# Performance work log

Measured on AMD Instinct MI355X. Metric: run time of the kernel, lower is better.

## Reference

```python
import jax, jax.numpy as jnp
import numpy as np

N_NODES = 100000
N_EDGES = 1600000
IN_F = 128
N_HEADS = 8
HEAD_D = 8  # n_hidden // n_heads = 64 // 8
NEG_SLOPE = 0.2


def setup_inputs() -> dict:
    key = jax.random.key(0)
    k1, k2, k3, k4, k5 = jax.random.split(key, 5)
    vert = jax.random.normal(k1, (N_NODES, IN_F), dtype=jnp.float32)
    edge = jax.random.randint(k2, (2, N_EDGES), 0, N_NODES, dtype=jnp.int64)
    scale_w = 1.0 / np.sqrt(IN_F)
    W = jax.random.normal(k3, (IN_F, N_HEADS, HEAD_D), dtype=jnp.float32) * scale_w
    scale_a = 1.0 / np.sqrt(HEAD_D)
    a_src = jax.random.normal(k4, (N_HEADS, HEAD_D), dtype=jnp.float32) * scale_a
    a_dst = jax.random.normal(k5, (N_HEADS, HEAD_D), dtype=jnp.float32) * scale_a
    return {"vert": vert, "edge": edge, "W": W, "a_src": a_src, "a_dst": a_dst}


def reference(vert, edge, W, a_src, a_dst):
    # Per-head linear projection: [N, H, D]
    g = jnp.einsum('nf,fhd->nhd', vert, W)
    src, dst = edge[0], edge[1]
    # Decomposed attention logits: e_ij = LeakyReLU(a_src.g_i + a_dst.g_j)
    e_s = jnp.sum(g * a_src[None], axis=-1)  # [N, H]
    e_d = jnp.sum(g * a_dst[None], axis=-1)  # [N, H]
    scores = jax.nn.leaky_relu(e_s[src] + e_d[dst], NEG_SLOPE)  # [E, H]
    # Segment softmax over incoming edges of each destination node
    m = jax.ops.segment_max(scores, dst, num_segments=N_NODES)  # [N, H]
    m = jnp.where(jnp.isneginf(m), 0.0, m)
    ex = jnp.exp(scores - m[dst])  # [E, H]
    denom = jax.ops.segment_sum(ex, dst, num_segments=N_NODES)  # [N, H]
    alpha = ex / jnp.maximum(denom[dst], 1e-16)  # [E, H]
    # Weighted message aggregation: scatter-add alpha * g[src] into dst
    msg = alpha[:, :, None] * g[src]  # [E, H, D]
    agg = jax.ops.segment_sum(msg, dst, num_segments=N_NODES)  # [N, H, D]
    out = agg.reshape(N_NODES, N_HEADS * HEAD_D)  # concat heads
    # GAT_DE trailing ELU (dropout=0.0 -> identity)
    return jax.nn.elu(out)
```

## Files before the change

kernel.cpp:

```cpp
#include <hip/hip_runtime.h>
#include <hip/hip_bf16.h>
#include <math.h>

#define N_NODES 100000
#define N_EDGES 1600000
#define IN_F    128
#define NH      8
#define HD      8
#define HID     64
#define NEG_SLOPE 0.2f

#define BSH   5
#define BSZ   32
#define NBK   3125
#define BCAPG 704
#define BCAP  832
#define NBPJ  782
#define NPB   160
#define EPB   10000

typedef short bf16x8 __attribute__((ext_vector_type(8)));
typedef float f32x4  __attribute__((ext_vector_type(4)));

static __device__ __forceinline__ unsigned short f2bf(float x) {
    __hip_bfloat16 h = __float2bfloat16(x);
    return *(unsigned short*)&h;
}

__global__ __launch_bounds__(512) void fused_pp_kernel(
    const float* __restrict__ vert, const float* __restrict__ W,
    const float* __restrict__ a_src, const float* __restrict__ a_dst,
    __hip_bfloat16* __restrict__ gb, float* __restrict__ es, float* __restrict__ ed,
    const int* __restrict__ edge, int* __restrict__ gcnt,
    unsigned int* __restrict__ packed)
{
    __shared__ __align__(16) char smem[25088];
    const int tid = threadIdx.x;

    if (blockIdx.x < NBPJ) {
        unsigned short* b_lds = (unsigned short*)smem;
        const int nbeg = blockIdx.x * 128;
        const int lane = tid & 63, wv = tid >> 6;
        const int mn   = lane & 15, quad = lane >> 4;

        for (int idx = tid; idx < 128 * 16; idx += 512) {
            const int f = idx >> 4, cq = idx & 15;
            const float4 w = *(const float4*)(W + f * 64 + cq * 4);
            const int kc = f >> 5, q = (f >> 3) & 3, j = f & 7;
            const float wf[4] = {w.x, w.y, w.z, w.w};
            #pragma unroll
            for (int i = 0; i < 4; ++i) {
                const int col = cq * 4 + i;
                b_lds[(col >> 4) * 2048 + kc * 512 + q * 128 + (col & 15) * 8 + j]
                    = f2bf(wf[i]);
            }
        }
        for (int idx = tid; idx < 128 * 8; idx += 512) {
            const int f = idx >> 3, h = idx & 7;
            const float4 wa = *(const float4*)(W + f * 64 + h * 8);
            const float4 wb = *(const float4*)(W + f * 64 + h * 8 + 4);
            const float4 sa = *(const float4*)(a_src + h * 8);
            const float4 sb = *(const float4*)(a_src + h * 8 + 4);
            const float4 da = *(const float4*)(a_dst + h * 8);
            const float4 db = *(const float4*)(a_dst + h * 8 + 4);
            float esv = fmaf(wa.x, sa.x, fmaf(wa.y, sa.y, fmaf(wa.z, sa.z,
                        fmaf(wa.w, sa.w, fmaf(wb.x, sb.x, fmaf(wb.y, sb.y,
                        fmaf(wb.z, sb.z, wb.w * sb.w)))))));
            float edv = fmaf(wa.x, da.x, fmaf(wa.y, da.y, fmaf(wa.z, da.z,
                        fmaf(wa.w, da.w, fmaf(wb.x, db.x, fmaf(wb.y, db.y,
                        fmaf(wb.z, db.z, wb.w * db.w)))))));
            const int kc = f >> 5, q = (f >> 3) & 3, j = f & 7;
            b_lds[4 * 2048 + kc * 512 + q * 128 + h * 8 + j]       = f2bf(esv);
            b_lds[4 * 2048 + kc * 512 + q * 128 + (8 + h) * 8 + j] = f2bf(edv);
        }

        const int row = nbeg + wv * 16 + mn;
        bf16x8 afr[4];
        #pragma unroll
        for (int kc = 0; kc < 4; ++kc) {
            float4 p = make_float4(0.f, 0.f, 0.f, 0.f);
            float4 q4 = make_float4(0.f, 0.f, 0.f, 0.f);
            if (row < N_NODES) {
                const float* rp = vert + (size_t)row * IN_F + kc * 32 + quad * 8;
                p  = *(const float4*)rp;
                q4 = *(const float4*)(rp + 4);
            }
            bf16x8 a;
            a[0] = (short)f2bf(p.x);  a[1] = (short)f2bf(p.y);
            a[2] = (short)f2bf(p.z);  a[3] = (short)f2bf(p.w);
            a[4] = (short)f2bf(q4.x); a[5] = (short)f2bf(q4.y);
            a[6] = (short)f2bf(q4.z); a[7] = (short)f2bf(q4.w);
            afr[kc] = a;
        }
        __syncthreads();

        const unsigned short* bbase = b_lds + quad * 128 + mn * 8;
        f32x4 acc[5];
        #pragma unroll
        for (int c = 0; c < 5; ++c) acc[c] = (f32x4){0.f, 0.f, 0.f, 0.f};
        #pragma unroll
        for (int kc = 0; kc < 4; ++kc) {
            #pragma unroll
            for (int c = 0; c < 5; ++c) {
                const bf16x8 bfr = *(const bf16x8*)(bbase + c * 2048 + kc * 512);
                acc[c] = __builtin_amdgcn_mfma_f32_16x16x32_bf16(afr[kc], bfr, acc[c], 0, 0, 0);
            }
        }
        __syncthreads();

        unsigned short* gl = (unsigned short*)smem + wv * 1024;
        float* lesd = (float*)(smem + 16384) + wv * 256;
        #pragma unroll
        for (int c = 0; c < 4; ++c)
            #pragma unroll
            for (int r = 0; r < 4; ++r)
                gl[(quad * 4 + r) * 64 + c * 16 + mn] = f2bf(acc[c][r]);
        {
            float* dst = (mn < 8) ? (lesd + mn) : (lesd + 128 + (mn - 8));
            #pragma unroll
            for (int r = 0; r < 4; ++r) dst[(quad * 4 + r) * 8] = acc[4][r];
        }
        {
            const int row2 = lane >> 2, part = lane & 3;
            const int node = nbeg + wv * 16 + row2;
            if (node < N_NODES) {
                const uint4* sp = (const uint4*)(gl + row2 * 64 + part * 16);
                *(uint4*)((unsigned short*)gb + (size_t)node * HID + part * 16) = sp[0];
                *(uint4*)((unsigned short*)gb + (size_t)node * HID + part * 16 + 8) = sp[1];
            }
        }
        {
            const int nl = lane >> 2, h2 = (lane & 3) * 2;
            const int node = nbeg + wv * 16 + nl;
            if (node < N_NODES) {
                *(float2*)(es + node * NH + h2) = *(const float2*)(lesd + nl * 8 + h2);
                *(float2*)(ed + node * NH + h2) = *(const float2*)(lesd + 128 + nl * 8 + h2);
            }
        }
    } else {
        int* lh    = (int*)smem;
        int* lbase = (int*)(smem + 12544);
        const int pb = blockIdx.x - NBPJ;

        for (int i = tid; i < NBK; i += 512) lh[i] = 0;
        __syncthreads();
        const int4* src4 = (const int4*)(edge + pb * EPB);
        const int4* dst4 = (const int4*)(edge + N_EDGES + pb * EPB);
        for (int t = tid; t < EPB / 4; t += 512) {
            const int4 d = dst4[t];
            atomicAdd(&lh[d.x >> BSH], 1);
            atomicAdd(&lh[d.y >> BSH], 1);
            atomicAdd(&lh[d.z >> BSH], 1);
            atomicAdd(&lh[d.w >> BSH], 1);
        }
        __syncthreads();
        for (int i = tid; i < NBK; i += 512) {
            const int c = lh[i];
            lbase[i] = c ? (i * BCAPG + atomicAdd(&gcnt[i], c)) : 0;
            lh[i] = 0;
        }
        __syncthreads();
        for (int t = tid; t < EPB / 4; t += 512) {
            const int4 s = src4[t];
            const int4 d = dst4[t];
            int bk, pos;
            bk = d.x >> BSH; pos = min(lbase[bk] + atomicAdd(&lh[bk], 1), NBK * BCAPG - 1);
            packed[pos] = ((unsigned)s.x << BSH) | (d.x & (BSZ - 1));
            bk = d.y >> BSH; pos = min(lbase[bk] + atomicAdd(&lh[bk], 1), NBK * BCAPG - 1);
            packed[pos] = ((unsigned)s.y << BSH) | (d.y & (BSZ - 1));
            bk = d.z >> BSH; pos = min(lbase[bk] + atomicAdd(&lh[bk], 1), NBK * BCAPG - 1);
            packed[pos] = ((unsigned)s.z << BSH) | (d.z & (BSZ - 1));
            bk = d.w >> BSH; pos = min(lbase[bk] + atomicAdd(&lh[bk], 1), NBK * BCAPG - 1);
            packed[pos] = ((unsigned)s.w << BSH) | (d.w & (BSZ - 1));
        }
    }
}

__global__ __launch_bounds__(256) void p2agg_kernel(
    const int* __restrict__ gcnt, const unsigned int* __restrict__ packed,
    const unsigned short* __restrict__ gb, const float* __restrict__ es,
    const float* __restrict__ ed, float* __restrict__ out)
{
    __shared__ unsigned int epk[BCAP];
    __shared__ unsigned int ssrt[BCAP];
    __shared__ int ldeg[BSZ], loffs[BSZ];
    __shared__ float led[BSZ * NH];

    const int tid  = threadIdx.x;
    const int b    = blockIdx.x;
    const int nbeg = b << BSH;
    const int ebase = b * BCAPG;
    const int ecnt  = min(gcnt[b], BCAP);

    if (tid < BSZ) ldeg[tid] = 0;
    for (int i = tid; i < BSZ * NH; i += 256) led[i] = ed[nbeg * NH + i];
    __syncthreads();

    for (int i = tid; i < ecnt; i += 256) {
        const unsigned int p = packed[ebase + i];
        epk[i] = p;
        atomicAdd(&ldeg[p & (BSZ - 1)], 1);
    }
    __syncthreads();

    if (tid < BSZ) {
        int v = ldeg[tid];
        #pragma unroll
        for (int off = 1; off < BSZ; off <<= 1) {
            const int t = __shfl_up(v, off, 64);
            if (tid >= off) v += t;
        }
        loffs[tid] = v - ldeg[tid];
    }
    __syncthreads();

    for (int i = tid; i < ecnt; i += 256) {
        const unsigned int p = epk[i];
        const int pos = atomicAdd(&loffs[p & (BSZ - 1)], 1);
        ssrt[pos] = p >> BSH;
    }
    __syncthreads();

    const int lane  = tid & 63;
    const int wv    = tid >> 6;
    const int h     = lane >> 3;
    const int d8    = lane & 7;
    const int c2    = lane & 31;
    const int khalf = lane >> 5;
    const int bpbase = ((c2 >> 2) * 8 + khalf) * 4;
    const unsigned* gbw = (const unsigned*)gb;

    for (int n = wv; n < BSZ; n += 4) {
        const int node = nbeg + n;
        const float edh = led[n * NH + h];
        const int end = loffs[n];
        const int beg = end - ldeg[n];
        float l = 0.f, acc0 = 0.f, acc1 = 0.f;
        for (int i = beg; i < end; i += 8) {
            const int idx = min(i + d8, end - 1);
            const int sd  = (int)ssrt[idx];
            float sc = es[sd * NH + h] + edh;
            sc = fmaxf(sc, sc * NEG_SLOPE);
            const float pd = (i + d8 < end) ? __expf(sc) : 0.f;
            #pragma unroll
            for (int s = 0; s < 4; ++s) {
                const int a  = bpbase + s * 8;
                const int se = __builtin_amdgcn_ds_bpermute(a, sd);
                const float pe = __uint_as_float((unsigned)
                    __builtin_amdgcn_ds_bpermute(a, __float_as_int(pd)));
                const unsigned gu = gbw[(unsigned)(se * 32 + c2)];
                acc0 = fmaf(pe, __uint_as_float(gu << 16), acc0);
                acc1 = fmaf(pe, __uint_as_float(gu & 0xFFFF0000u), acc1);
                l += pe;
            }
        }
        l    += __shfl_xor(l, 32);
        acc0 += __shfl_xor(acc0, 32);
        acc1 += __shfl_xor(acc1, 32);
        const float rl = 1.f / fmaxf(l, 1e-16f);
        float o0 = acc0 * rl, o1 = acc1 * rl;
        o0 = (o0 > 0.f) ? o0 : expm1f(o0);
        o1 = (o1 > 0.f) ? o1 : expm1f(o1);
        const float ov = khalf ? o1 : o0;
        out[(size_t)node * HID + c2 * 2 + khalf] = ov;
    }
}

extern "C" void kernel_launch(void* const* d_in, const int* in_sizes, int n_in,
                              void* d_out, int out_size, void* d_ws, size_t ws_size,
                              hipStream_t stream)
{
    const float* vert  = (const float*)d_in[0];
    const int*   edge  = (const int*)  d_in[1];
    const float* W     = (const float*)d_in[2];
    const float* a_src = (const float*)d_in[3];
    const float* a_dst = (const float*)d_in[4];
    float* out = (float*)d_out;

    char* ws = (char*)d_ws;
    __hip_bfloat16* gb     = (__hip_bfloat16*)(ws);
    float*          es     = (float*)(ws + 12800000);
    float*          ed     = (float*)(ws + 16000000);
    unsigned int*   packed = (unsigned int*)(ws + 19200000);
    int*            gcnt   = (int*)(ws + 28000000);

    hipMemsetAsync(gcnt, 0, NBK * sizeof(int), stream);

    fused_pp_kernel<<<NBPJ + NPB, 512, 0, stream>>>(
        vert, W, a_src, a_dst, gb, es, ed, edge, gcnt, packed);
    p2agg_kernel<<<NBK, 256, 0, stream>>>(gcnt, packed, (const unsigned short*)gb, es, ed, out);
}
```

Before: 186.7 us.

## Precompute bf16 weight tiles once, pad LDS staging, precompute fp16 edge exps in aggregation

```diff
diff --git a/kernel.cpp b/kernel.cpp
--- a/kernel.cpp
+++ b/kernel.cpp
@@ -1,5 +1,6 @@
 #include <hip/hip_runtime.h>
 #include <hip/hip_bf16.h>
+#include <hip/hip_fp16.h>
 #include <math.h>
 
 #define N_NODES 100000
@@ -27,14 +28,57 @@
     return *(unsigned short*)&h;
 }
 
+__global__ __launch_bounds__(256) void prep_kernel(
+    const float* __restrict__ W, const float* __restrict__ a_src,
+    const float* __restrict__ a_dst, unsigned short* __restrict__ Bg,
+    int* __restrict__ gcnt)
+{
+    const int tid = threadIdx.x;
+    for (int i = blockIdx.x * 256 + tid; i < NBK; i += 16 * 256) gcnt[i] = 0;
+    if (blockIdx.x != 0) return;
+
+    __shared__ __align__(16) unsigned short bl[10240];
+    for (int idx = tid; idx < 128 * 16; idx += 256) {
+        const int f = idx >> 4, cq = idx & 15;
+        const float4 w = *(const float4*)(W + f * 64 + cq * 4);
+        const int kc = f >> 5, q = (f >> 3) & 3, j = f & 7;
+        const float wf[4] = {w.x, w.y, w.z, w.w};
+        #pragma unroll
+        for (int i = 0; i < 4; ++i) {
+            const int col = cq * 4 + i;
+            bl[(col >> 4) * 2048 + kc * 512 + q * 128 + (col & 15) * 8 + j] = f2bf(wf[i]);
+        }
+    }
+    for (int idx = tid; idx < 128 * 8; idx += 256) {
+        const int f = idx >> 3, h = idx & 7;
+        const float4 wa = *(const float4*)(W + f * 64 + h * 8);
+        const float4 wb = *(const float4*)(W + f * 64 + h * 8 + 4);
+        const float4 sa = *(const float4*)(a_src + h * 8);
+        const float4 sb = *(const float4*)(a_src + h * 8 + 4);
+        const float4 da = *(const float4*)(a_dst + h * 8);
+        const float4 db = *(const float4*)(a_dst + h * 8 + 4);
+        float esv = fmaf(wa.x, sa.x, fmaf(wa.y, sa.y, fmaf(wa.z, sa.z,
+                    fmaf(wa.w, sa.w, fmaf(wb.x, sb.x, fmaf(wb.y, sb.y,
+                    fmaf(wb.z, sb.z, wb.w * sb.w)))))));
+        float edv = fmaf(wa.x, da.x, fmaf(wa.y, da.y, fmaf(wa.z, da.z,
+                    fmaf(wa.w, da.w, fmaf(wb.x, db.x, fmaf(wb.y, db.y,
+                    fmaf(wb.z, db.z, wb.w * db.w)))))));
+        const int kc = f >> 5, q = (f >> 3) & 3, j = f & 7;
+        bl[4 * 2048 + kc * 512 + q * 128 + h * 8 + j]       = f2bf(esv);
+        bl[4 * 2048 + kc * 512 + q * 128 + (8 + h) * 8 + j] = f2bf(edv);
+    }
+    __syncthreads();
+    for (int idx = tid; idx < 1280; idx += 256)
+        ((uint4*)Bg)[idx] = ((const uint4*)bl)[idx];
+}
+
 __global__ __launch_bounds__(512) void fused_pp_kernel(
-    const float* __restrict__ vert, const float* __restrict__ W,
-    const float* __restrict__ a_src, const float* __restrict__ a_dst,
+    const float* __restrict__ vert, const unsigned short* __restrict__ Bg,
     __hip_bfloat16* __restrict__ gb, float* __restrict__ es, float* __restrict__ ed,
     const int* __restrict__ edge, int* __restrict__ gcnt,
     unsigned int* __restrict__ packed)
 {
-    __shared__ __align__(16) char smem[25088];
+    __shared__ __align__(16) char smem[28672];
     const int tid = threadIdx.x;
 
     if (blockIdx.x < NBPJ) {
@@ -43,36 +87,8 @@
         const int lane = tid & 63, wv = tid >> 6;
         const int mn   = lane & 15, quad = lane >> 4;
 
-        for (int idx = tid; idx < 128 * 16; idx += 512) {
-            const int f = idx >> 4, cq = idx & 15;
-            const float4 w = *(const float4*)(W + f * 64 + cq * 4);
-            const int kc = f >> 5, q = (f >> 3) & 3, j = f & 7;
-            const float wf[4] = {w.x, w.y, w.z, w.w};
-            #pragma unroll
-            for (int i = 0; i < 4; ++i) {
-                const int col = cq * 4 + i;
-                b_lds[(col >> 4) * 2048 + kc * 512 + q * 128 + (col & 15) * 8 + j]
-                    = f2bf(wf[i]);
-            }
-        }
-        for (int idx = tid; idx < 128 * 8; idx += 512) {
-            const int f = idx >> 3, h = idx & 7;
-            const float4 wa = *(const float4*)(W + f * 64 + h * 8);
-            const float4 wb = *(const float4*)(W + f * 64 + h * 8 + 4);
-            const float4 sa = *(const float4*)(a_src + h * 8);
-            const float4 sb = *(const float4*)(a_src + h * 8 + 4);
-            const float4 da = *(const float4*)(a_dst + h * 8);
-            const float4 db = *(const float4*)(a_dst + h * 8 + 4);
-            float esv = fmaf(wa.x, sa.x, fmaf(wa.y, sa.y, fmaf(wa.z, sa.z,
-                        fmaf(wa.w, sa.w, fmaf(wb.x, sb.x, fmaf(wb.y, sb.y,
-                        fmaf(wb.z, sb.z, wb.w * sb.w)))))));
-            float edv = fmaf(wa.x, da.x, fmaf(wa.y, da.y, fmaf(wa.z, da.z,
-                        fmaf(wa.w, da.w, fmaf(wb.x, db.x, fmaf(wb.y, db.y,
-                        fmaf(wb.z, db.z, wb.w * db.w)))))));
-            const int kc = f >> 5, q = (f >> 3) & 3, j = f & 7;
-            b_lds[4 * 2048 + kc * 512 + q * 128 + h * 8 + j]       = f2bf(esv);
-            b_lds[4 * 2048 + kc * 512 + q * 128 + (8 + h) * 8 + j] = f2bf(edv);
-        }
+        for (int idx = tid; idx < 1280; idx += 512)
+            *(uint4*)(smem + idx * 16) = ((const uint4*)Bg)[idx];
 
         const int row = nbeg + wv * 16 + mn;
         bf16x8 afr[4];
@@ -108,23 +124,24 @@
         }
         __syncthreads();
 
-        unsigned short* gl = (unsigned short*)smem + wv * 1024;
-        float* lesd = (float*)(smem + 16384) + wv * 256;
+        unsigned short* gl = (unsigned short*)smem + wv * 1152;
+        float* lesd = (float*)(smem + 18432) + wv * 320;
         #pragma unroll
         for (int c = 0; c < 4; ++c)
             #pragma unroll
             for (int r = 0; r < 4; ++r)
-                gl[(quad * 4 + r) * 64 + c * 16 + mn] = f2bf(acc[c][r]);
+                gl[(quad * 4 + r) * 72 + c * 16 + mn] = f2bf(acc[c][r]);
         {
-            float* dst = (mn < 8) ? (lesd + mn) : (lesd + 128 + (mn - 8));
+            float* dst = (mn < 8) ? (lesd + mn) : (lesd + 160 + (mn - 8));
             #pragma unroll
-            for (int r = 0; r < 4; ++r) dst[(quad * 4 + r) * 8] = acc[4][r];
-        }
+            for (int r = 0; r < 4; ++r) dst[(quad * 4 + r) * 10] = acc[4][r];
+        }
+        __syncthreads();
         {
             const int row2 = lane >> 2, part = lane & 3;
             const int node = nbeg + wv * 16 + row2;
             if (node < N_NODES) {
-                const uint4* sp = (const uint4*)(gl + row2 * 64 + part * 16);
+                const uint4* sp = (const uint4*)(gl + row2 * 72 + part * 16);
                 *(uint4*)((unsigned short*)gb + (size_t)node * HID + part * 16) = sp[0];
                 *(uint4*)((unsigned short*)gb + (size_t)node * HID + part * 16 + 8) = sp[1];
             }
@@ -133,8 +150,8 @@
             const int nl = lane >> 2, h2 = (lane & 3) * 2;
             const int node = nbeg + wv * 16 + nl;
             if (node < N_NODES) {
-                *(float2*)(es + node * NH + h2) = *(const float2*)(lesd + nl * 8 + h2);
-                *(float2*)(ed + node * NH + h2) = *(const float2*)(lesd + 128 + nl * 8 + h2);
+                *(float2*)(es + node * NH + h2) = *(const float2*)(lesd + nl * 10 + h2);
+                *(float2*)(ed + node * NH + h2) = *(const float2*)(lesd + 160 + nl * 10 + h2);
             }
         }
     } else {
@@ -181,10 +198,11 @@
     const unsigned short* __restrict__ gb, const float* __restrict__ es,
     const float* __restrict__ ed, float* __restrict__ out)
 {
-    __shared__ unsigned int epk[BCAP];
     __shared__ unsigned int ssrt[BCAP];
+    __shared__ __align__(16) unsigned short pexp[BCAP * 8];
     __shared__ int ldeg[BSZ], loffs[BSZ];
-    __shared__ float led[BSZ * NH];
+    __shared__ __align__(16) float led[BSZ * NH];
+    unsigned int* epk = (unsigned int*)pexp;
 
     const int tid  = threadIdx.x;
     const int b    = blockIdx.x;
@@ -217,37 +235,53 @@
     for (int i = tid; i < ecnt; i += 256) {
         const unsigned int p = epk[i];
         const int pos = atomicAdd(&loffs[p & (BSZ - 1)], 1);
-        ssrt[pos] = p >> BSH;
+        ssrt[pos] = p;
+    }
+    __syncthreads();
+
+    for (int i = tid; i < ecnt; i += 256) {
+        const unsigned p = ssrt[i];
+        const int src = (int)(p >> BSH), dl = (int)(p & (BSZ - 1));
+        const float4 e0 = *(const float4*)(es + (size_t)src * NH);
+        const float4 e1 = *(const float4*)(es + (size_t)src * NH + 4);
+        const float4 l0 = *(const float4*)(led + dl * NH);
+        const float4 l1 = *(const float4*)(led + dl * NH + 4);
+        float s[8] = {e0.x + l0.x, e0.y + l0.y, e0.z + l0.z, e0.w + l0.w,
+                      e1.x + l1.x, e1.y + l1.y, e1.z + l1.z, e1.w + l1.w};
+        #pragma unroll
+        for (int k = 0; k < 8; ++k)
+            s[k] = __expf(fmaxf(s[k], s[k] * NEG_SLOPE));
+        __half2 h01 = __floats2half2_rn(s[0], s[1]);
+        __half2 h23 = __floats2half2_rn(s[2], s[3]);
+        __half2 h45 = __floats2half2_rn(s[4], s[5]);
+        __half2 h67 = __floats2half2_rn(s[6], s[7]);
+        uint4 w;
+        w.x = *(unsigned*)&h01; w.y = *(unsigned*)&h23;
+        w.z = *(unsigned*)&h45; w.w = *(unsigned*)&h67;
+        *(uint4*)(pexp + i * 8) = w;
     }
     __syncthreads();
 
     const int lane  = tid & 63;
     const int wv    = tid >> 6;
-    const int h     = lane >> 3;
-    const int d8    = lane & 7;
     const int c2    = lane & 31;
     const int khalf = lane >> 5;
-    const int bpbase = ((c2 >> 2) * 8 + khalf) * 4;
+    const int h     = c2 >> 2;
     const unsigned* gbw = (const unsigned*)gb;
 
     for (int n = wv; n < BSZ; n += 4) {
-        const int node = nbeg + n;
-        const float edh = led[n * NH + h];
         const int end = loffs[n];
         const int beg = end - ldeg[n];
         float l = 0.f, acc0 = 0.f, acc1 = 0.f;
         for (int i = beg; i < end; i += 8) {
-            const int idx = min(i + d8, end - 1);
-            const int sd  = (int)ssrt[idx];
-            float sc = es[sd * NH + h] + edh;
-            sc = fmaxf(sc, sc * NEG_SLOPE);
-            const float pd = (i + d8 < end) ? __expf(sc) : 0.f;
             #pragma unroll
             for (int s = 0; s < 4; ++s) {
-                const int a  = bpbase + s * 8;
-                const int se = __builtin_amdgcn_ds_bpermute(a, sd);
-                const float pe = __uint_as_float((unsigned)
-                    __builtin_amdgcn_ds_bpermute(a, __float_as_int(pd)));
+                const int e  = i + 2 * s + khalf;
+                const int ec = min(e, end - 1);
+                const unsigned pw = ssrt[ec];
+                const int se = (int)(pw >> BSH);
+                float pe = __half2float(*(const __half*)(pexp + ec * 8 + h));
+                pe = (e < end) ? pe : 0.f;
                 const unsigned gu = gbw[(unsigned)(se * 32 + c2)];
                 acc0 = fmaf(pe, __uint_as_float(gu << 16), acc0);
                 acc1 = fmaf(pe, __uint_as_float(gu & 0xFFFF0000u), acc1);
@@ -262,7 +296,7 @@
         o0 = (o0 > 0.f) ? o0 : expm1f(o0);
         o1 = (o1 > 0.f) ? o1 : expm1f(o1);
         const float ov = khalf ? o1 : o0;
-        out[(size_t)node * HID + c2 * 2 + khalf] = ov;
+        out[(size_t)(nbeg + n) * HID + c2 * 2 + khalf] = ov;
     }
 }
 
@@ -283,10 +317,10 @@
     float*          ed     = (float*)(ws + 16000000);
     unsigned int*   packed = (unsigned int*)(ws + 19200000);
     int*            gcnt   = (int*)(ws + 28000000);
-
-    hipMemsetAsync(gcnt, 0, NBK * sizeof(int), stream);
-
+    unsigned short* Bg     = (unsigned short*)(ws + 28012544);
+
+    prep_kernel<<<16, 256, 0, stream>>>(W, a_src, a_dst, Bg, gcnt);
     fused_pp_kernel<<<NBPJ + NPB, 512, 0, stream>>>(
-        vert, W, a_src, a_dst, gb, es, ed, edge, gcnt, packed);
+        vert, Bg, gb, es, ed, edge, gcnt, packed);
     p2agg_kernel<<<NBK, 256, 0, stream>>>(gcnt, packed, (const unsigned short*)gb, es, ed, out);
 }
```

Result: no change. 185.6 us (-0.6%).
